# Kernel optimization log

Measured on AMD Instinct MI355X. Metric: run time of the kernel, lower is better.

The kernel has to match this reference:

```python
import jax, jax.numpy as jnp
import numpy as np

B, D, H = 128, 256, 512  # batch, input_size, hidden_size; 2 hidden layers
ORDER = 'A'
EPS = 1e-12


def _masks():
    # Standard MADE sequential degrees: inputs 1..D (reversed for order 'B'),
    # hidden degrees cycle over 1..D-1. Hidden mask: >=, output mask: > (strict).
    din = np.arange(1, D + 1) if ORDER == 'A' else np.arange(D, 0, -1)
    dh = (np.arange(H) % (D - 1)) + 1
    m0 = (dh[:, None] >= din[None, :]).astype(np.float32)  # [H, D]
    m1 = (dh[:, None] >= dh[None, :]).astype(np.float32)   # [H, H]
    mo = (din[:, None] > dh[None, :]).astype(np.float32)   # [D, H]
    return jnp.asarray(m0), jnp.asarray(m1), jnp.asarray(mo)


def _made(y, W0, b0, W1, b1, Wo, bo, masks):
    m0, m1, mo = masks
    h = jax.nn.elu(y @ (W0 * m0).T + b0)   # [B, H]
    h = jax.nn.elu(h @ (W1 * m1).T + b1)   # [B, H]
    return h @ (Wo * mo).T + bo            # [B, D]


def setup_inputs() -> dict:
    key = jax.random.key(0)
    ks = jax.random.split(key, 13)
    s_in, s_h = 1.0 / np.sqrt(D), 1.0 / np.sqrt(H)

    def p(k, shape, s):
        return (jax.random.normal(k, shape, jnp.float32) * s).astype(jnp.float32)

    return {
        'x': jax.random.normal(ks[0], (B, D), jnp.float32),
        'mu_W0': p(ks[1], (H, D), s_in), 'mu_b0': jnp.zeros((H,), jnp.float32),
        'mu_W1': p(ks[2], (H, H), s_h),  'mu_b1': jnp.zeros((H,), jnp.float32),
        'mu_Wo': p(ks[3], (D, H), s_h),  'mu_bo': jnp.zeros((D,), jnp.float32),
        'lv_W0': p(ks[4], (H, D), s_in), 'lv_b0': jnp.zeros((H,), jnp.float32),
        'lv_W1': p(ks[5], (H, H), s_h),  'lv_b1': jnp.zeros((H,), jnp.float32),
        'lv_Wo': p(ks[6], (D, H), s_h),  'lv_bo': jnp.zeros((D,), jnp.float32),
    }


def reference(x, mu_W0, mu_b0, mu_W1, mu_b1, mu_Wo, mu_bo,
              lv_W0, lv_b0, lv_W1, lv_b1, lv_Wo, lv_bo):
    masks = _masks()
    idx = jnp.arange(D) if ORDER == 'A' else jnp.arange(D - 1, -1, -1)

    def step(carry, i):
        y, _ = carry
        mu = _made(y, mu_W0, mu_b0, mu_W1, mu_b1, mu_Wo, mu_bo, masks)
        logstd = 0.5 * _made(y, lv_W0, lv_b0, lv_W1, lv_b1, lv_Wo, lv_bo, masks)
        new_col = (x[:, i] - mu[:, i]) / (jnp.exp(logstd[:, i]) + EPS)
        y = y.at[:, i].set(new_col)
        return (y, logstd), None

    init = (jnp.zeros_like(x), jnp.zeros_like(x))
    (y, logstd), _ = jax.lax.scan(step, init, idx)
    return y, logstd.sum(axis=1)
```

## Files before the change

kernel.cpp:

```cpp
#include <hip/hip_runtime.h>

#define DD 256
#define HH 512
#define BB 128
#define TS 4096

#define WAITVM(N) asm volatile("s_waitcnt vmcnt(" #N ")" ::: "memory")
#define PIN4(v) asm volatile("" :: "v"((v).x), "v"((v).y), "v"((v).z), "v"((v).w))

__device__ __forceinline__ float elu_f(float x) {
    return x > 0.f ? x : (__expf(x) - 1.f);
}
__device__ __forceinline__ float rlf(float v, int l) {
    return __uint_as_float(__builtin_amdgcn_readlane(__float_as_uint(v), (unsigned)l));
}
__device__ __forceinline__ float f4c(const float4& v, int r) {
    return r == 0 ? v.x : r == 1 ? v.y : r == 2 ? v.z : v.w;
}

__device__ __forceinline__ int pmap(int h) {
    if (h == 510) return 255;
    if (h == 511) return 511;
    return (h < 255) ? (4 * (h & 63) + (h >> 6))
                     : (256 + 4 * ((h - 255) & 63) + ((h - 255) >> 6));
}
__device__ __forceinline__ int p4map(int j) {
    return 4 * (j & 63) + (j >> 6);
}
__device__ __forceinline__ int w1base(int hp) {
    return (hp <= 254) ? hp * TS
         : (hp <= 509) ? (hp - 255) * TS + 1024
         : 255 * TS + ((hp == 510) ? 0 : 1024);
}
__device__ __forceinline__ int wobase(int hp) {
    return (hp <= 254) ? hp * TS + 3072
         : (hp <= 509) ? (hp - 255) * TS + 3584
         : 255 * TS + ((hp == 510) ? 2048 : 2560);
}

__global__ __launch_bounds__(256) void prep(
    const float* __restrict__ w0m_, const float* __restrict__ w0l_,
    const float* __restrict__ w1m_, const float* __restrict__ w1l_,
    const float* __restrict__ wom_, const float* __restrict__ wol_,
    float* __restrict__ tape)
{
    __shared__ float tm[32][33], tl[32][33];
    const int tx = threadIdx.x & 31, ty = threadIdx.x >> 5;
    const unsigned b = blockIdx.x;

    if (b < 256) {
        const int h0 = (int)(b >> 4) << 5, hp0 = (int)(b & 15) << 5;
        #pragma unroll
        for (int j = 0; j < 4; ++j) {
            int r = ty + 8 * j;
            tm[r][tx] = w1m_[(h0 + r) * HH + hp0 + tx];
            tl[r][tx] = w1l_[(h0 + r) * HH + hp0 + tx];
        }
        __syncthreads();
        #pragma unroll
        for (int j = 0; j < 4; ++j) {
            int hp = hp0 + ty + 8 * j;
            int h  = h0 + tx;
            int dh_h = (h <= 254) ? h + 1 : (h <= 509 ? h - 254 : h - 509);
            int dh_p = (hp <= 254) ? hp + 1 : (hp <= 509 ? hp - 254 : hp - 509);
            float mask = (dh_h >= dh_p) ? 1.f : 0.f;
            int base = w1base(hp), p = pmap(h);
            tape[base + p]       = mask * tm[tx][ty + 8 * j];
            tape[base + 512 + p] = mask * tl[tx][ty + 8 * j];
        }
    } else if (b < 384) {
        const int b2 = (int)b - 256;
        const int h0 = (b2 >> 3) << 5, i0 = (b2 & 7) << 5;
        #pragma unroll
        for (int j = 0; j < 4; ++j) {
            int r = ty + 8 * j;
            tm[r][tx] = w0m_[(h0 + r) * DD + i0 + tx];
            tl[r][tx] = w0l_[(h0 + r) * DD + i0 + tx];
        }
        __syncthreads();
        #pragma unroll
        for (int j = 0; j < 4; ++j) {
            int i = i0 + ty + 8 * j;
            int h = h0 + tx;
            int p = pmap(h);
            tape[i * TS + 2048 + p] = tm[tx][ty + 8 * j];
            tape[i * TS + 2560 + p] = tl[tx][ty + 8 * j];
        }
    } else {
        const int b3 = (int)b - 384;
        const int j0 = (b3 >> 4) << 5, hp0 = (b3 & 15) << 5;
        #pragma unroll
        for (int j = 0; j < 4; ++j) {
            int r = ty + 8 * j;
            tm[r][tx] = wom_[(j0 + r) * HH + hp0 + tx];
            tl[r][tx] = wol_[(j0 + r) * HH + hp0 + tx];
        }
        __syncthreads();
        #pragma unroll
        for (int j = 0; j < 4; ++j) {
            int hp = hp0 + ty + 8 * j;
            int jj = j0 + tx;
            int base = wobase(hp), p = p4map(jj);
            tape[base + p]       = tm[tx][ty + 8 * j];
            tape[base + 256 + p] = tl[tx][ty + 8 * j];
        }
    }
}

__device__ __forceinline__ void stage16(const float* g, float* l, int lane) {
    #pragma unroll
    for (int k = 0; k < 16; ++k) {
        __builtin_amdgcn_global_load_lds(
            (const __attribute__((address_space(1))) void*)(g + 256 * k + 4 * lane),
            (__attribute__((address_space(3))) void*)(l + 256 * k),
            16, 0, 0);
    }
}

struct MSet { float4 w8, w9, w0, w4, w1, w5, w12, w14; };
struct LSet { float4 w10, w11, w2, w6, w3, w7, w13, w15; };

__device__ __forceinline__ void rdM(MSet& S, const float* b, int lane) {
    const float4* p = (const float4*)b;
    S.w8  = p[64 * 8 + lane];  S.w9  = p[64 * 9 + lane];
    S.w0  = p[64 * 0 + lane];  S.w4  = p[64 * 4 + lane];
    S.w1  = p[64 * 1 + lane];  S.w5  = p[64 * 5 + lane];
    S.w12 = p[64 * 12 + lane]; S.w14 = p[64 * 14 + lane];
}
__device__ __forceinline__ void rdL(LSet& S, const float* b, int lane) {
    const float4* p = (const float4*)b;
    S.w10 = p[64 * 10 + lane]; S.w11 = p[64 * 11 + lane];
    S.w2  = p[64 * 2 + lane];  S.w6  = p[64 * 6 + lane];
    S.w3  = p[64 * 3 + lane];  S.w7  = p[64 * 7 + lane];
    S.w13 = p[64 * 13 + lane]; S.w15 = p[64 * 15 + lane];
}
__device__ __forceinline__ void pinM(const MSet& S) {
    PIN4(S.w8); PIN4(S.w9); PIN4(S.w0); PIN4(S.w4);
    PIN4(S.w1); PIN4(S.w5); PIN4(S.w12); PIN4(S.w14);
}
__device__ __forceinline__ void pinL(const LSet& S) {
    PIN4(S.w10); PIN4(S.w11); PIN4(S.w2); PIN4(S.w6);
    PIN4(S.w3); PIN4(S.w7); PIN4(S.w13); PIN4(S.w15);
}

template<int Q, int EX>
__device__ __forceinline__ void stepM(
    int tl, int lane, float v, const MSet& S,
    float (&a0m)[8], float (&a1m)[8], float (&Rm)[4], float (&yv)[4],
    const float4& exA, const float4& exB, const float4& exW)
{
    yv[Q] = (lane == tl) ? v : yv[Q];

    #pragma unroll
    for (int r = Q; r < 4; ++r) {
        a0m[r]     += v * f4c(S.w8, r);
        a0m[4 + r] += v * f4c(S.w9, r);
    }
    float p0 = elu_f(rlf(a0m[Q], tl));
    float p1 = elu_f(rlf(a0m[4 + Q], tl));
    float p2 = 0.f;
    if (EX) p2 = elu_f(rlf(a0m[EX == 1 ? 3 : 7], 63));

    #pragma unroll
    for (int r = Q; r < 4; ++r) {
        a1m[r]     += f4c(S.w0, r) * p0 + f4c(S.w4, r) * p1;
        a1m[4 + r] += f4c(S.w1, r) * p0 + f4c(S.w5, r) * p1;
    }
    if (EX) {
        #pragma unroll
        for (int r = 0; r < 4; ++r) {
            a1m[r]     += f4c(exA, r) * p2;
            a1m[4 + r] += f4c(exB, r) * p2;
        }
    }

    float q0 = elu_f(rlf(a1m[Q], tl));
    float q1 = elu_f(rlf(a1m[4 + Q], tl));
    float q2 = 0.f;
    if (EX) q2 = elu_f(rlf(a1m[EX == 1 ? 3 : 7], 63));

    #pragma unroll
    for (int r = Q; r < 4; ++r)
        Rm[r] += f4c(S.w12, r) * q0 + f4c(S.w14, r) * q1;
    if (EX) {
        #pragma unroll
        for (int r = 0; r < 4; ++r) Rm[r] += f4c(exW, r) * q2;
    }
}

template<int Q, int EX>
__device__ __forceinline__ void stepL(
    int tl, int lane, float v, const LSet& S,
    float (&a0l)[8], float (&a1l)[8], float (&Rl)[4],
    const float4& exA, const float4& exB, const float4& exW)
{
    #pragma unroll
    for (int r = Q; r < 4; ++r) {
        a0l[r]     += v * f4c(S.w10, r);
        a0l[4 + r] += v * f4c(S.w11, r);
    }
    float p0 = elu_f(rlf(a0l[Q], tl));
    float p1 = elu_f(rlf(a0l[4 + Q], tl));
    float p2 = 0.f;
    if (EX) p2 = elu_f(rlf(a0l[EX == 1 ? 3 : 7], 63));

    #pragma unroll
    for (int r = Q; r < 4; ++r) {
        a1l[r]     += f4c(S.w2, r) * p0 + f4c(S.w6, r) * p1;
        a1l[4 + r] += f4c(S.w3, r) * p0 + f4c(S.w7, r) * p1;
    }
    if (EX) {
        #pragma unroll
        for (int r = 0; r < 4; ++r) {
            a1l[r]     += f4c(exA, r) * p2;
            a1l[4 + r] += f4c(exB, r) * p2;
        }
    }

    float q0 = elu_f(rlf(a1l[Q], tl));
    float q1 = elu_f(rlf(a1l[4 + Q], tl));
    float q2 = 0.f;
    if (EX) q2 = elu_f(rlf(a1l[EX == 1 ? 3 : 7], 63));

    #pragma unroll
    for (int r = Q; r < 4; ++r)
        Rl[r] += f4c(S.w13, r) * q0 + f4c(S.w15, r) * q1;
    if (EX) {
        #pragma unroll
        for (int r = 0; r < 4; ++r) Rl[r] += f4c(exW, r) * q2;
    }
}

__global__ __launch_bounds__(192, 1) void made_main(
    const float* __restrict__ x,
    const float* __restrict__ mu_b0, const float* __restrict__ mu_b1,
    const float* __restrict__ mu_bo,
    const float* __restrict__ lv_b0, const float* __restrict__ lv_b1,
    const float* __restrict__ lv_bo,
    const float* __restrict__ tape,
    float* __restrict__ out)
{
    __shared__ __align__(16) float buf[4][TS];
    __shared__ __align__(8) float exch[2][2];
    const int row  = blockIdx.x;
    const int lane = threadIdx.x & 63;
    const int wid  = threadIdx.x >> 6;

    const float4 d4 = make_float4(0.f, 0.f, 0.f, 0.f);

    if (wid == 2) {
        #pragma unroll
        for (int g = 0; g < 3; ++g)
            stage16(tape + (size_t)g * TS, &buf[g][0], lane);
        #pragma unroll 1
        for (int t = 0; t < 255; ++t) {
            if (t < 253) { WAITVM(16); } else { WAITVM(0); }
            __builtin_amdgcn_s_barrier();
            __builtin_amdgcn_sched_barrier(0);
            int g = t + 3;
            if (g < 255)
                stage16(tape + (size_t)g * TS, &buf[g & 3][0], lane);
        }
        __builtin_amdgcn_s_barrier();
        return;
    }

    const float4* a4 = (const float4*)(tape + 255 * TS);

    if (wid == 0) {
        float a0m[8], a1m[8], Rm[4], yv[4], xv[4], bmv[4];
        #pragma unroll
        for (int r = 0; r < 4; ++r) {
            a0m[r]     = mu_b0[lane + 64 * r];
            a0m[4 + r] = mu_b0[255 + lane + 64 * r];
            a1m[r]     = mu_b1[lane + 64 * r];
            a1m[4 + r] = mu_b1[255 + lane + 64 * r];
            Rm[r] = 0.f; yv[r] = 0.f;
            xv[r]  = x[row * DD + 64 * r + lane];
            bmv[r] = mu_bo[64 * r + lane];
        }
        if (lane == 63) {
            a0m[3] = mu_b0[510]; a0m[7] = mu_b0[511];
            a1m[3] = mu_b1[510]; a1m[7] = mu_b1[511];
        }
        float4 e510A = a4[lane],       e510B = a4[64 + lane];
        float4 e511A = a4[256 + lane], e511B = a4[320 + lane];
        float4 wo510 = a4[512 + lane], wo511 = a4[640 + lane];

        MSet A, B;

        {
            float d0 = xv[0] - (Rm[0] + bmv[0]);
            if (lane == 0) exch[0][0] = d0;
        }

        __syncthreads();
        {
            rdM(A, &buf[0][0], lane);
            rdM(B, &buf[1][0], lane);
            float2 ds0 = *(const float2*)&exch[0][0];
            float v0 = ds0.x * ds0.y;
            stepM<0, 1>(0, lane, v0, A, a0m, a1m, Rm, yv, e510A, e510B, wo510);
            float dn = xv[0] - (Rm[0] + bmv[0]);
            if (lane == 1) exch[1][0] = dn;
            pinM(B);
        }
        __syncthreads();
        {
            rdM(A, &buf[2][0], lane);
            float2 ds1 = *(const float2*)&exch[1][0];
            float v1 = ds1.x * ds1.y;
            stepM<0, 2>(1, lane, v1, B, a0m, a1m, Rm, yv, e511A, e511B, wo511);
            float dn = xv[0] - (Rm[0] + bmv[0]);
            if (lane == 2) exch[0][0] = dn;
            pinM(A);
        }

#define MBODY(Q, tt, Qn, tn, SC, SN, PREF)                                    \
    {                                                                         \
        __syncthreads();                                                      \
        if (PREF) rdM(SN, &buf[((tt) + 1) & 3][0], lane);                     \
        float2 ds_ = *(const float2*)&exch[(tt) & 1][0];                      \
        float v_ = ds_.x * ds_.y;                                             \
        stepM<Q, 0>((tt) - 64 * (Q), lane, v_, SC, a0m, a1m, Rm, yv,          \
                    d4, d4, d4);                                              \
        float dn_ = xv[Qn] - (Rm[Qn] + bmv[Qn]);                              \
        if (lane == (tn)) exch[((tt) + 1) & 1][0] = dn_;                      \
        if (PREF) pinM(SN);                                                   \
    }
        #pragma unroll 1
        for (int t = 2; t < 62; t += 2) {
            MBODY(0, t, 0, t + 1, A, B, 1)
            MBODY(0, t + 1, 0, t + 2, B, A, 1)
        }
        MBODY(0, 62, 0, 63, A, B, 1)
        MBODY(0, 63, 1, 0, B, A, 1)
        #pragma unroll 1
        for (int t = 64; t < 126; t += 2) {
            MBODY(1, t, 1, t - 63, A, B, 1)
            MBODY(1, t + 1, 1, t - 62, B, A, 1)
        }
        MBODY(1, 126, 1, 63, A, B, 1)
        MBODY(1, 127, 2, 0, B, A, 1)
        #pragma unroll 1
        for (int t = 128; t < 190; t += 2) {
            MBODY(2, t, 2, t - 127, A, B, 1)
            MBODY(2, t + 1, 2, t - 126, B, A, 1)
        }
        MBODY(2, 190, 2, 63, A, B, 1)
        MBODY(2, 191, 3, 0, B, A, 1)
        #pragma unroll 1
        for (int t = 192; t < 252; t += 2) {
            MBODY(3, t, 3, t - 191, A, B, 1)
            MBODY(3, t + 1, 3, t - 190, B, A, 1)
        }
        MBODY(3, 252, 3, 61, A, B, 1)
        MBODY(3, 253, 3, 62, B, A, 1)
        MBODY(3, 254, 3, 63, A, B, 0)
#undef MBODY

        __syncthreads();
        {
            float2 dsF = *(const float2*)&exch[1][0];
            yv[3] = (lane == 63) ? dsF.x * dsF.y : yv[3];
        }
        #pragma unroll
        for (int r = 0; r < 4; ++r) out[row * DD + 64 * r + lane] = yv[r];
    } else {
        float a0l[8], a1l[8], Rl[4], xv[4], blv[4];
        #pragma unroll
        for (int r = 0; r < 4; ++r) {
            a0l[r]     = lv_b0[lane + 64 * r];
            a0l[4 + r] = lv_b0[255 + lane + 64 * r];
            a1l[r]     = lv_b1[lane + 64 * r];
            a1l[4 + r] = lv_b1[255 + lane + 64 * r];
            Rl[r] = 0.f;
            xv[r]  = x[row * DD + 64 * r + lane];
            blv[r] = lv_bo[64 * r + lane];
        }
        if (lane == 63) {
            a0l[3] = lv_b0[510]; a0l[7] = lv_b0[511];
            a1l[3] = lv_b1[510]; a1l[7] = lv_b1[511];
        }
        float4 e510A = a4[128 + lane], e510B = a4[192 + lane];
        float4 e511A = a4[384 + lane], e511B = a4[448 + lane];
        float4 wo510 = a4[576 + lane], wo511 = a4[704 + lane];

        LSet A, B;
        float ls_part = 0.f;

        {
            float ls0 = 0.5f * (Rl[0] + blv[0]);
            float s0  = __fdividef(1.f, __expf(ls0) + 1e-12f);
            ls_part += (lane == 0) ? ls0 : 0.f;
            if (lane == 0) exch[0][1] = s0;
        }

        __syncthreads();
        {
            rdL(A, &buf[0][0], lane);
            rdL(B, &buf[1][0], lane);
            float2 ds0 = *(const float2*)&exch[0][0];
            float v0 = ds0.x * ds0.y;
            stepL<0, 1>(0, lane, v0, A, a0l, a1l, Rl, e510A, e510B, wo510);
            float lsn = 0.5f * (Rl[0] + blv[0]);
            float sn  = __fdividef(1.f, __expf(lsn) + 1e-12f);
            ls_part += (lane == 1) ? lsn : 0.f;
            if (lane == 1) exch[1][1] = sn;
            pinL(B);
        }
        __syncthreads();
        {
            rdL(A, &buf[2][0], lane);
            float2 ds1 = *(const float2*)&exch[1][0];
            float v1 = ds1.x * ds1.y;
            stepL<0, 2>(1, lane, v1, B, a0l, a1l, Rl, e511A, e511B, wo511);
            float lsn = 0.5f * (Rl[0] + blv[0]);
            float sn  = __fdividef(1.f, __expf(lsn) + 1e-12f);
            ls_part += (lane == 2) ? lsn : 0.f;
            if (lane == 2) exch[0][1] = sn;
            pinL(A);
        }

#define LBODY(Q, tt, Qn, tn, SC, SN, PREF)                                    \
    {                                                                         \
        __syncthreads();                                                      \
        if (PREF) rdL(SN, &buf[((tt) + 1) & 3][0], lane);                     \
        float2 ds_ = *(const float2*)&exch[(tt) & 1][0];                      \
        float v_ = ds_.x * ds_.y;                                             \
        stepL<Q, 0>((tt) - 64 * (Q), lane, v_, SC, a0l, a1l, Rl, d4, d4, d4); \
        float lsn_ = 0.5f * (Rl[Qn] + blv[Qn]);                               \
        float sn_  = __fdividef(1.f, __expf(lsn_) + 1e-12f);                  \
        ls_part += (lane == (tn)) ? lsn_ : 0.f;                               \
        if (lane == (tn)) exch[((tt) + 1) & 1][1] = sn_;                      \
        if (PREF) pinL(SN);                                                   \
    }
        #pragma unroll 1
        for (int t = 2; t < 62; t += 2) {
            LBODY(0, t, 0, t + 1, A, B, 1)
            LBODY(0, t + 1, 0, t + 2, B, A, 1)
        }
        LBODY(0, 62, 0, 63, A, B, 1)
        LBODY(0, 63, 1, 0, B, A, 1)
        #pragma unroll 1
        for (int t = 64; t < 126; t += 2) {
            LBODY(1, t, 1, t - 63, A, B, 1)
            LBODY(1, t + 1, 1, t - 62, B, A, 1)
        }
        LBODY(1, 126, 1, 63, A, B, 1)
        LBODY(1, 127, 2, 0, B, A, 1)
        #pragma unroll 1
        for (int t = 128; t < 190; t += 2) {
            LBODY(2, t, 2, t - 127, A, B, 1)
            LBODY(2, t + 1, 2, t - 126, B, A, 1)
        }
        LBODY(2, 190, 2, 63, A, B, 1)
        LBODY(2, 191, 3, 0, B, A, 1)
        #pragma unroll 1
        for (int t = 192; t < 252; t += 2) {
            LBODY(3, t, 3, t - 191, A, B, 1)
            LBODY(3, t + 1, 3, t - 190, B, A, 1)
        }
        LBODY(3, 252, 3, 61, A, B, 1)
        LBODY(3, 253, 3, 62, B, A, 1)
        LBODY(3, 254, 3, 63, A, B, 0)
#undef LBODY

        __syncthreads();
        #pragma unroll
        for (int off = 32; off; off >>= 1)
            ls_part += __shfl_down(ls_part, off);
        if (lane == 0) out[BB * DD + row] = ls_part;
    }
}

extern "C" void kernel_launch(void* const* d_in, const int* in_sizes, int n_in,
                              void* d_out, int out_size, void* d_ws, size_t ws_size,
                              hipStream_t stream) {
    const float* x     = (const float*)d_in[0];
    const float* mu_W0 = (const float*)d_in[1];
    const float* mu_b0 = (const float*)d_in[2];
    const float* mu_W1 = (const float*)d_in[3];
    const float* mu_b1 = (const float*)d_in[4];
    const float* mu_Wo = (const float*)d_in[5];
    const float* mu_bo = (const float*)d_in[6];
    const float* lv_W0 = (const float*)d_in[7];
    const float* lv_b0 = (const float*)d_in[8];
    const float* lv_W1 = (const float*)d_in[9];
    const float* lv_b1 = (const float*)d_in[10];
    const float* lv_Wo = (const float*)d_in[11];
    const float* lv_bo = (const float*)d_in[12];

    float* tape = (float*)d_ws;

    prep<<<512, 256, 0, stream>>>(mu_W0, lv_W0, mu_W1, lv_W1, mu_Wo, lv_Wo, tape);
    made_main<<<BB, 192, 0, stream>>>(x, mu_b0, mu_b1, mu_bo,
                                      lv_b0, lv_b1, lv_bo, tape, (float*)d_out);
}
```

Baseline: 154.6 us.

## Replace LDS staging warp with direct global-to-register weight prefetch

```diff
diff --git a/kernel.cpp b/kernel.cpp
--- a/kernel.cpp
+++ b/kernel.cpp
@@ -6,7 +6,8 @@
 #define TS 4096
 
 #define WAITVM(N) asm volatile("s_waitcnt vmcnt(" #N ")" ::: "memory")
-#define PIN4(v) asm volatile("" :: "v"((v).x), "v"((v).y), "v"((v).z), "v"((v).w))
+#define WAITLGKM0() asm volatile("s_waitcnt lgkmcnt(0)" ::: "memory")
+#define SBAR() do { __builtin_amdgcn_s_barrier(); __builtin_amdgcn_sched_barrier(0); } while (0)
 
 __device__ __forceinline__ float elu_f(float x) {
     return x > 0.f ? x : (__expf(x) - 1.f);
@@ -107,40 +108,22 @@
     }
 }
 
-__device__ __forceinline__ void stage16(const float* g, float* l, int lane) {
-    #pragma unroll
-    for (int k = 0; k < 16; ++k) {
-        __builtin_amdgcn_global_load_lds(
-            (const __attribute__((address_space(1))) void*)(g + 256 * k + 4 * lane),
-            (__attribute__((address_space(3))) void*)(l + 256 * k),
-            16, 0, 0);
-    }
-}
-
 struct MSet { float4 w8, w9, w0, w4, w1, w5, w12, w14; };
 struct LSet { float4 w10, w11, w2, w6, w3, w7, w13, w15; };
 
-__device__ __forceinline__ void rdM(MSet& S, const float* b, int lane) {
-    const float4* p = (const float4*)b;
+__device__ __forceinline__ void ldM(MSet& S, const float* g, int lane) {
+    const float4* p = (const float4*)g;
     S.w8  = p[64 * 8 + lane];  S.w9  = p[64 * 9 + lane];
     S.w0  = p[64 * 0 + lane];  S.w4  = p[64 * 4 + lane];
     S.w1  = p[64 * 1 + lane];  S.w5  = p[64 * 5 + lane];
     S.w12 = p[64 * 12 + lane]; S.w14 = p[64 * 14 + lane];
 }
-__device__ __forceinline__ void rdL(LSet& S, const float* b, int lane) {
-    const float4* p = (const float4*)b;
+__device__ __forceinline__ void ldL(LSet& S, const float* g, int lane) {
+    const float4* p = (const float4*)g;
     S.w10 = p[64 * 10 + lane]; S.w11 = p[64 * 11 + lane];
     S.w2  = p[64 * 2 + lane];  S.w6  = p[64 * 6 + lane];
     S.w3  = p[64 * 3 + lane];  S.w7  = p[64 * 7 + lane];
     S.w13 = p[64 * 13 + lane]; S.w15 = p[64 * 15 + lane];
-}
-__device__ __forceinline__ void pinM(const MSet& S) {
-    PIN4(S.w8); PIN4(S.w9); PIN4(S.w0); PIN4(S.w4);
-    PIN4(S.w1); PIN4(S.w5); PIN4(S.w12); PIN4(S.w14);
-}
-__device__ __forceinline__ void pinL(const LSet& S) {
-    PIN4(S.w10); PIN4(S.w11); PIN4(S.w2); PIN4(S.w6);
-    PIN4(S.w3); PIN4(S.w7); PIN4(S.w13); PIN4(S.w15);
 }
 
 template<int Q, int EX>
@@ -231,7 +214,7 @@
     }
 }
 
-__global__ __launch_bounds__(192, 1) void made_main(
+__global__ __launch_bounds__(128, 1) void made_main(
     const float* __restrict__ x,
     const float* __restrict__ mu_b0, const float* __restrict__ mu_b1,
     const float* __restrict__ mu_bo,
@@ -240,31 +223,12 @@
     const float* __restrict__ tape,
     float* __restrict__ out)
 {
-    __shared__ __align__(16) float buf[4][TS];
     __shared__ __align__(8) float exch[2][2];
     const int row  = blockIdx.x;
     const int lane = threadIdx.x & 63;
     const int wid  = threadIdx.x >> 6;
 
     const float4 d4 = make_float4(0.f, 0.f, 0.f, 0.f);
-
-    if (wid == 2) {
-        #pragma unroll
-        for (int g = 0; g < 3; ++g)
-            stage16(tape + (size_t)g * TS, &buf[g][0], lane);
-        #pragma unroll 1
-        for (int t = 0; t < 255; ++t) {
-            if (t < 253) { WAITVM(16); } else { WAITVM(0); }
-            __builtin_amdgcn_s_barrier();
-            __builtin_amdgcn_sched_barrier(0);
-            int g = t + 3;
-            if (g < 255)
-                stage16(tape + (size_t)g * TS, &buf[g & 3][0], lane);
-        }
-        __builtin_amdgcn_s_barrier();
-        return;
-    }
-
     const float4* a4 = (const float4*)(tape + 255 * TS);
 
     if (wid == 0) {
@@ -287,79 +251,85 @@
         float4 e511A = a4[256 + lane], e511B = a4[320 + lane];
         float4 wo510 = a4[512 + lane], wo511 = a4[640 + lane];
 
-        MSet A, B;
+        MSet WA, WB;
+        ldM(WA, tape + 0 * TS, lane);
+        ldM(WB, tape + 1 * TS, lane);
 
         {
             float d0 = xv[0] - (Rm[0] + bmv[0]);
             if (lane == 0) exch[0][0] = d0;
         }
-
-        __syncthreads();
-        {
-            rdM(A, &buf[0][0], lane);
-            rdM(B, &buf[1][0], lane);
-            float2 ds0 = *(const float2*)&exch[0][0];
-            float v0 = ds0.x * ds0.y;
-            stepM<0, 1>(0, lane, v0, A, a0m, a1m, Rm, yv, e510A, e510B, wo510);
-            float dn = xv[0] - (Rm[0] + bmv[0]);
-            if (lane == 1) exch[1][0] = dn;
-            pinM(B);
-        }
-        __syncthreads();
-        {
-            rdM(A, &buf[2][0], lane);
-            float2 ds1 = *(const float2*)&exch[1][0];
-            float v1 = ds1.x * ds1.y;
-            stepM<0, 2>(1, lane, v1, B, a0m, a1m, Rm, yv, e511A, e511B, wo511);
-            float dn = xv[0] - (Rm[0] + bmv[0]);
-            if (lane == 2) exch[0][0] = dn;
-            pinM(A);
-        }
-
-#define MBODY(Q, tt, Qn, tn, SC, SN, PREF)                                    \
+        WAITVM(8);
+        WAITLGKM0();
+        SBAR();
+
+        {
+            float2 ds_ = *(const float2*)&exch[0][0];
+            float v_ = ds_.x * ds_.y;
+            stepM<0, 1>(0, lane, v_, WA, a0m, a1m, Rm, yv, e510A, e510B, wo510);
+            ldM(WA, tape + 2 * TS, lane);
+            float dn_ = xv[0] - (Rm[0] + bmv[0]);
+            if (lane == 1) exch[1][0] = dn_;
+            WAITVM(8);
+            WAITLGKM0();
+            SBAR();
+        }
+        {
+            float2 ds_ = *(const float2*)&exch[1][0];
+            float v_ = ds_.x * ds_.y;
+            stepM<0, 2>(1, lane, v_, WB, a0m, a1m, Rm, yv, e511A, e511B, wo511);
+            ldM(WB, tape + 3 * TS, lane);
+            float dn_ = xv[0] - (Rm[0] + bmv[0]);
+            if (lane == 2) exch[0][0] = dn_;
+            WAITVM(8);
+            WAITLGKM0();
+            SBAR();
+        }
+
+#define MBODY(Q, tt, Qn, tn, SC)                                              \
     {                                                                         \
-        __syncthreads();                                                      \
-        if (PREF) rdM(SN, &buf[((tt) + 1) & 3][0], lane);                     \
         float2 ds_ = *(const float2*)&exch[(tt) & 1][0];                      \
         float v_ = ds_.x * ds_.y;                                             \
         stepM<Q, 0>((tt) - 64 * (Q), lane, v_, SC, a0m, a1m, Rm, yv,          \
                     d4, d4, d4);                                              \
+        if ((tt) + 2 < 255) ldM(SC, tape + (size_t)((tt) + 2) * TS, lane);    \
         float dn_ = xv[Qn] - (Rm[Qn] + bmv[Qn]);                              \
         if (lane == (tn)) exch[((tt) + 1) & 1][0] = dn_;                      \
-        if (PREF) pinM(SN);                                                   \
+        if ((tt) < 253) { WAITVM(8); } else { WAITVM(0); }                    \
+        WAITLGKM0();                                                          \
+        SBAR();                                                               \
     }
         #pragma unroll 1
         for (int t = 2; t < 62; t += 2) {
-            MBODY(0, t, 0, t + 1, A, B, 1)
-            MBODY(0, t + 1, 0, t + 2, B, A, 1)
-        }
-        MBODY(0, 62, 0, 63, A, B, 1)
-        MBODY(0, 63, 1, 0, B, A, 1)
+            MBODY(0, t, 0, t + 1, WA)
+            MBODY(0, t + 1, 0, t + 2, WB)
+        }
+        MBODY(0, 62, 0, 63, WA)
+        MBODY(0, 63, 1, 0, WB)
         #pragma unroll 1
         for (int t = 64; t < 126; t += 2) {
-            MBODY(1, t, 1, t - 63, A, B, 1)
-            MBODY(1, t + 1, 1, t - 62, B, A, 1)
-        }
-        MBODY(1, 126, 1, 63, A, B, 1)
-        MBODY(1, 127, 2, 0, B, A, 1)
+            MBODY(1, t, 1, t - 63, WA)
+            MBODY(1, t + 1, 1, t - 62, WB)
+        }
+        MBODY(1, 126, 1, 63, WA)
+        MBODY(1, 127, 2, 0, WB)
         #pragma unroll 1
         for (int t = 128; t < 190; t += 2) {
-            MBODY(2, t, 2, t - 127, A, B, 1)
-            MBODY(2, t + 1, 2, t - 126, B, A, 1)
-        }
-        MBODY(2, 190, 2, 63, A, B, 1)
-        MBODY(2, 191, 3, 0, B, A, 1)
+            MBODY(2, t, 2, t - 127, WA)
+            MBODY(2, t + 1, 2, t - 126, WB)
+        }
+        MBODY(2, 190, 2, 63, WA)
+        MBODY(2, 191, 3, 0, WB)
         #pragma unroll 1
         for (int t = 192; t < 252; t += 2) {
-            MBODY(3, t, 3, t - 191, A, B, 1)
-            MBODY(3, t + 1, 3, t - 190, B, A, 1)
-        }
-        MBODY(3, 252, 3, 61, A, B, 1)
-        MBODY(3, 253, 3, 62, B, A, 1)
-        MBODY(3, 254, 3, 63, A, B, 0)
+            MBODY(3, t, 3, t - 191, WA)
+            MBODY(3, t + 1, 3, t - 190, WB)
+        }
+        MBODY(3, 252, 3, 61, WA)
+        MBODY(3, 253, 3, 62, WB)
+        MBODY(3, 254, 3, 63, WA)
 #undef MBODY
 
-        __syncthreads();
         {
             float2 dsF = *(const float2*)&exch[1][0];
             yv[3] = (lane == 63) ? dsF.x * dsF.y : yv[3];
@@ -386,87 +356,93 @@
         float4 e511A = a4[384 + lane], e511B = a4[448 + lane];
         float4 wo510 = a4[576 + lane], wo511 = a4[704 + lane];
 
-        LSet A, B;
+        LSet WA, WB;
+        ldL(WA, tape + 0 * TS, lane);
+        ldL(WB, tape + 1 * TS, lane);
+
         float ls_part = 0.f;
-
         {
             float ls0 = 0.5f * (Rl[0] + blv[0]);
             float s0  = __fdividef(1.f, __expf(ls0) + 1e-12f);
             ls_part += (lane == 0) ? ls0 : 0.f;
             if (lane == 0) exch[0][1] = s0;
         }
-
-        __syncthreads();
-        {
-            rdL(A, &buf[0][0], lane);
-            rdL(B, &buf[1][0], lane);
-            float2 ds0 = *(const float2*)&exch[0][0];
-            float v0 = ds0.x * ds0.y;
-            stepL<0, 1>(0, lane, v0, A, a0l, a1l, Rl, e510A, e510B, wo510);
-            float lsn = 0.5f * (Rl[0] + blv[0]);
-            float sn  = __fdividef(1.f, __expf(lsn) + 1e-12f);
-            ls_part += (lane == 1) ? lsn : 0.f;
-            if (lane == 1) exch[1][1] = sn;
-            pinL(B);
-        }
-        __syncthreads();
-        {
-            rdL(A, &buf[2][0], lane);
-            float2 ds1 = *(const float2*)&exch[1][0];
-            float v1 = ds1.x * ds1.y;
-            stepL<0, 2>(1, lane, v1, B, a0l, a1l, Rl, e511A, e511B, wo511);
-            float lsn = 0.5f * (Rl[0] + blv[0]);
-            float sn  = __fdividef(1.f, __expf(lsn) + 1e-12f);
-            ls_part += (lane == 2) ? lsn : 0.f;
-            if (lane == 2) exch[0][1] = sn;
-            pinL(A);
-        }
-
-#define LBODY(Q, tt, Qn, tn, SC, SN, PREF)                                    \
+        WAITVM(8);
+        WAITLGKM0();
+        SBAR();
+
+        {
+            float2 ds_ = *(const float2*)&exch[0][0];
+            float v_ = ds_.x * ds_.y;
+            stepL<0, 1>(0, lane, v_, WA, a0l, a1l, Rl, e510A, e510B, wo510);
+            ldL(WA, tape + 2 * TS, lane);
+            float lsn_ = 0.5f * (Rl[0] + blv[0]);
+            float sn_  = __fdividef(1.f, __expf(lsn_) + 1e-12f);
+            ls_part += (lane == 1) ? lsn_ : 0.f;
+            if (lane == 1) exch[1][1] = sn_;
+            WAITVM(8);
+            WAITLGKM0();
+            SBAR();
+        }
+        {
+            float2 ds_ = *(const float2*)&exch[1][0];
+            float v_ = ds_.x * ds_.y;
+            stepL<0, 2>(1, lane, v_, WB, a0l, a1l, Rl, e511A, e511B, wo511);
+            ldL(WB, tape + 3 * TS, lane);
+            float lsn_ = 0.5f * (Rl[0] + blv[0]);
+            float sn_  = __fdividef(1.f, __expf(lsn_) + 1e-12f);
+            ls_part += (lane == 2) ? lsn_ : 0.f;
+            if (lane == 2) exch[0][1] = sn_;
+            WAITVM(8);
+            WAITLGKM0();
+            SBAR();
+        }
+
+#define LBODY(Q, tt, Qn, tn, SC)                                              \
     {                                                                         \
-        __syncthreads();                                                      \
-        if (PREF) rdL(SN, &buf[((tt) + 1) & 3][0], lane);                     \
         float2 ds_ = *(const float2*)&exch[(tt) & 1][0];                      \
         float v_ = ds_.x * ds_.y;                                             \
         stepL<Q, 0>((tt) - 64 * (Q), lane, v_, SC, a0l, a1l, Rl, d4, d4, d4); \
+        if ((tt) + 2 < 255) ldL(SC, tape + (size_t)((tt) + 2) * TS, lane);    \
         float lsn_ = 0.5f * (Rl[Qn] + blv[Qn]);                               \
         float sn_  = __fdividef(1.f, __expf(lsn_) + 1e-12f);                  \
         ls_part += (lane == (tn)) ? lsn_ : 0.f;                               \
         if (lane == (tn)) exch[((tt) + 1) & 1][1] = sn_;                      \
-        if (PREF) pinL(SN);                                                   \
+        if ((tt) < 253) { WAITVM(8); } else { WAITVM(0); }                    \
+        WAITLGKM0();                                                          \
+        SBAR();                                                               \
     }
         #pragma unroll 1
         for (int t = 2; t < 62; t += 2) {
-            LBODY(0, t, 0, t + 1, A, B, 1)
-            LBODY(0, t + 1, 0, t + 2, B, A, 1)
-        }
-        LBODY(0, 62, 0, 63, A, B, 1)
-        LBODY(0, 63, 1, 0, B, A, 1)
+            LBODY(0, t, 0, t + 1, WA)
+            LBODY(0, t + 1, 0, t + 2, WB)
+        }
+        LBODY(0, 62, 0, 63, WA)
+        LBODY(0, 63, 1, 0, WB)
         #pragma unroll 1
         for (int t = 64; t < 126; t += 2) {
-            LBODY(1, t, 1, t - 63, A, B, 1)
-            LBODY(1, t + 1, 1, t - 62, B, A, 1)
-        }
-        LBODY(1, 126, 1, 63, A, B, 1)
-        LBODY(1, 127, 2, 0, B, A, 1)
+            LBODY(1, t, 1, t - 63, WA)
+            LBODY(1, t + 1, 1, t - 62, WB)
+        }
+        LBODY(1, 126, 1, 63, WA)
+        LBODY(1, 127, 2, 0, WB)
         #pragma unroll 1
         for (int t = 128; t < 190; t += 2) {
-            LBODY(2, t, 2, t - 127, A, B, 1)
-            LBODY(2, t + 1, 2, t - 126, B, A, 1)
-        }
-        LBODY(2, 190, 2, 63, A, B, 1)
-        LBODY(2, 191, 3, 0, B, A, 1)
+            LBODY(2, t, 2, t - 127, WA)
+            LBODY(2, t + 1, 2, t - 126, WB)
+        }
+        LBODY(2, 190, 2, 63, WA)
+        LBODY(2, 191, 3, 0, WB)
         #pragma unroll 1
         for (int t = 192; t < 252; t += 2) {
-            LBODY(3, t, 3, t - 191, A, B, 1)
-            LBODY(3, t + 1, 3, t - 190, B, A, 1)
-        }
-        LBODY(3, 252, 3, 61, A, B, 1)
-        LBODY(3, 253, 3, 62, B, A, 1)
-        LBODY(3, 254, 3, 63, A, B, 0)
+            LBODY(3, t, 3, t - 191, WA)
+            LBODY(3, t + 1, 3, t - 190, WB)
+        }
+        LBODY(3, 252, 3, 61, WA)
+        LBODY(3, 253, 3, 62, WB)
+        LBODY(3, 254, 3, 63, WA)
 #undef LBODY
 
-        __syncthreads();
         #pragma unroll
         for (int off = 32; off; off >>= 1)
             ls_part += __shfl_down(ls_part, off);
@@ -494,6 +470,6 @@
     float* tape = (float*)d_ws;
 
     prep<<<512, 256, 0, stream>>>(mu_W0, lv_W0, mu_W1, lv_W1, mu_Wo, lv_Wo, tape);
-    made_main<<<BB, 192, 0, stream>>>(x, mu_b0, mu_b1, mu_bo,
+    made_main<<<BB, 128, 0, stream>>>(x, mu_b0, mu_b1, mu_bo,
                                       lv_b0, lv_b1, lv_bo, tape, (float*)d_out);
 }
```

After: 174.6 us. 1.13x slower.
